# Optimization experiments

Measured on AMD Instinct MI355X. Metric: run time of the kernel, lower is better.

The kernel has to match this reference:

```python
import jax, jax.numpy as jnp
import numpy as np

H = 4          # global_attention_heads
NL = 32        # num_landmark_tokens
STRIDE = 16    # landmark_stride
D = 3072       # hidden_size
HD = D // H    # head_dim = 768
SCALE = 1.0 / np.sqrt(HD).astype(np.float32)


def _landmark_indices(seq_len: int) -> jnp.ndarray:
    # torch: arange(0, seq_len, stride); if >NL, index with linspace(0, n-1, NL).long() (truncation)
    idx = np.arange(0, seq_len, STRIDE, dtype=np.int64)
    if len(idx) > NL:
        sel = np.linspace(0, len(idx) - 1, NL).astype(np.int64)  # truncates like torch long cast
        idx = idx[sel]
    return jnp.asarray(idx)


def _attn(q_in, kv_in, Wq, bq, Wk, bk, Wv, bv, Wo, bo):
    # shared QKV/O projections, standard multi-head attention q_in -> kv_in
    B, Lq, _ = q_in.shape
    Lk = kv_in.shape[1]
    Q = (q_in @ Wq + bq).reshape(B, Lq, H, HD)
    K = (kv_in @ Wk + bk).reshape(B, Lk, H, HD)
    V = (kv_in @ Wv + bv).reshape(B, Lk, H, HD)
    scores = jnp.einsum('bqhd,bkhd->bhqk', Q, K) * SCALE
    w = jax.nn.softmax(scores, axis=-1)  # dropout is identity in eval
    ctx = jnp.einsum('bhqk,bkhd->bqhd', w, V).reshape(B, Lq, D)
    return ctx @ Wo + bo


def setup_inputs() -> dict:
    key = jax.random.key(0)
    ks = jax.random.split(key, 10)
    B, S = 2, 8192
    s = 1.0 / np.sqrt(D).astype(np.float32)
    return {
        'hidden_states': jax.random.normal(ks[0], (B, S, D), jnp.float32),
        'landmark_emb': jax.random.normal(ks[1], (NL, D), jnp.float32),
        'Wq': jax.random.normal(ks[2], (D, D), jnp.float32) * s,
        'bq': jnp.zeros((D,), jnp.float32),
        'Wk': jax.random.normal(ks[3], (D, D), jnp.float32) * s,
        'bk': jnp.zeros((D,), jnp.float32),
        'Wv': jax.random.normal(ks[4], (D, D), jnp.float32) * s,
        'bv': jnp.zeros((D,), jnp.float32),
        'Wo': jax.random.normal(ks[5], (D, D), jnp.float32) * s,
        'bo': jnp.zeros((D,), jnp.float32),
    }


def reference(hidden_states, landmark_emb, Wq, bq, Wk, bk, Wv, bv, Wo, bo):
    B, S, _ = hidden_states.shape
    li = _landmark_indices(S)  # [NL], static
    # gather landmarks + learned landmark embeddings
    landmark_tokens = hidden_states[:, li, :] + landmark_emb[None]  # [B, NL, D]
    # all tokens attend to 32 landmarks
    global_out = _attn(hidden_states, landmark_tokens, Wq, bq, Wk, bk, Wv, bv, Wo, bo)  # [B,S,D]
    # landmarks attend to all tokens
    landmark_out = _attn(landmark_tokens, hidden_states, Wq, bq, Wk, bk, Wv, bv, Wo, bo)  # [B,NL,D]
    # scatter landmark outputs back (index_copy-style, replaces python loop)
    updated = hidden_states.at[:, li, :].set(landmark_out)
    return updated + global_out
```

## Files before the change

kernel.cpp:

```cpp
#include <hip/hip_runtime.h>
#include <stdint.h>

#define S_LEN   8192
#define DMODEL  3072
#define HDIM    768
#define NLM     32
#define MTOK    16384
#define MV      16448
#define MP      16512
#define NQKV    9216
#define KDIM    3072
#define NKT     48
#define MTILES  64
#define SCALE_F 0.036084391824351615f

#define OFF_A    ((size_t)0)
#define OFF_WT   ((size_t)101449728)
#define OFF_QKV  ((size_t)176947200)
#define OFF_CTX  ((size_t)480116736)
#define OFF_BCAT ((size_t)581566464)
#define OFF_PART ((size_t)581615616)
#define OFF_KT   (OFF_PART)
#define OFF_VT   (OFF_PART + 393216)
#define OFF_ML2  (OFF_PART + 786432)
#define OFF_LMP  (OFF_PART + 917504)
#define OFF_CP   (OFF_A)

#if defined(__has_builtin)
#if __has_builtin(__builtin_amdgcn_global_load_lds)
#define USE_GLL 1
#endif
#endif
#ifndef USE_GLL
#define USE_GLL 0
#endif

typedef __attribute__((ext_vector_type(8))) short bf8_t;
typedef __attribute__((ext_vector_type(4))) float f4_t;
typedef __attribute__((ext_vector_type(4))) short s4_t;
typedef __attribute__((ext_vector_type(4))) unsigned short us4_t;

__device__ __forceinline__ float b2f(unsigned short u) {
  unsigned x = ((unsigned)u) << 16;
  float f;
  __builtin_memcpy(&f, &x, 4);
  return f;
}
__device__ __forceinline__ unsigned short f2b(float f) {
  unsigned x;
  __builtin_memcpy(&x, &f, 4);
  x += 0x7fffu + ((x >> 16) & 1u);
  return (unsigned short)(x >> 16);
}
__device__ __forceinline__ void load12(const unsigned short* p, float* f) {
  s4_t v0 = *(const s4_t*)p;
  s4_t v1 = *(const s4_t*)(p + 4);
  s4_t v2 = *(const s4_t*)(p + 8);
#pragma unroll
  for (int e = 0; e < 4; ++e) {
    f[e]     = b2f((unsigned short)v0[e]);
    f[4 + e] = b2f((unsigned short)v1[e]);
    f[8 + e] = b2f((unsigned short)v2[e]);
  }
}
__device__ __forceinline__ void store12(unsigned short* p, const float* f) {
  us4_t a = {f2b(f[0]), f2b(f[1]), f2b(f[2]), f2b(f[3])};
  us4_t b = {f2b(f[4]), f2b(f[5]), f2b(f[6]), f2b(f[7])};
  us4_t c = {f2b(f[8]), f2b(f[9]), f2b(f[10]), f2b(f[11])};
  *(us4_t*)p = a;
  *(us4_t*)(p + 4) = b;
  *(us4_t*)(p + 8) = c;
}

__global__ __launch_bounds__(256) void build_bcat(const float* __restrict__ bq,
                                                  const float* __restrict__ bk,
                                                  const float* __restrict__ bv,
                                                  const float* __restrict__ bo,
                                                  float* __restrict__ bcat) {
  int n = blockIdx.x * 256 + threadIdx.x;
  float v = (n < 3072) ? bq[n] : (n < 6144) ? bk[n - 3072]
          : (n < 9216) ? bv[n - 6144] : bo[n - 9216];
  bcat[n] = v;
}

__global__ __launch_bounds__(256) void build_a(const float* __restrict__ hs,
                                               const float* __restrict__ lemb,
                                               unsigned short* __restrict__ A) {
  size_t idx = (size_t)blockIdx.x * 256 + threadIdx.x;
  size_t e = idx * 4;
  int row = (int)(e / DMODEL);
  int col = (int)(e - (size_t)row * DMODEL);
  f4_t v;
  if (row < MTOK) {
    v = *(const f4_t*)(hs + e);
  } else if (row < MV) {
    int r2 = row - MTOK;
    int b = r2 >> 5, j = r2 & 31;
    int sel = (j * 511) / 31;
    int li = sel * 16;
    f4_t a = *(const f4_t*)(hs + ((size_t)(b * S_LEN + li)) * DMODEL + col);
    f4_t c = *(const f4_t*)(lemb + (size_t)j * DMODEL + col);
    v = a + c;
  } else {
    v = (f4_t){0.f, 0.f, 0.f, 0.f};
  }
  us4_t o = {f2b(v[0]), f2b(v[1]), f2b(v[2]), f2b(v[3])};
  *(us4_t*)(A + e) = o;
}

__global__ __launch_bounds__(256) void wtrans4(const float* __restrict__ W0,
                                               const float* __restrict__ W1,
                                               const float* __restrict__ W2,
                                               const float* __restrict__ W3,
                                               unsigned short* __restrict__ Wt) {
  __shared__ float t[32][33];
  const float* Wsel[4] = {W0, W1, W2, W3};
  const float* W = Wsel[blockIdx.z];
  unsigned short* dst = Wt + (size_t)blockIdx.z * 3072 * KDIM;
  int n0 = blockIdx.x * 32, k0 = blockIdx.y * 32;
  int x = threadIdx.x, y = threadIdx.y;
#pragma unroll
  for (int i = 0; i < 4; ++i)
    t[y + i * 8][x] = W[(size_t)(k0 + y + i * 8) * DMODEL + n0 + x];
  __syncthreads();
#pragma unroll
  for (int i = 0; i < 4; ++i)
    dst[(size_t)(n0 + y + i * 8) * DMODEL + k0 + x] = f2b(t[x][y + i * 8]);
}

__global__ __launch_bounds__(256) void lm_gemm_part(const unsigned short* __restrict__ A64,
                                                    const unsigned short* __restrict__ Bt,
                                                    float* __restrict__ part,
                                                    int N) {
  int wid = blockIdx.x * 4 + (threadIdx.x >> 6);
  int lane = threadIdx.x & 63;
  int row16 = lane & 15, quad = lane >> 4;
  int strips = N >> 5;
  int ks = wid / strips;
  int n0 = (wid - ks * strips) * 32;

  f4_t acc[4][2];
#pragma unroll
  for (int mi = 0; mi < 4; ++mi) {
    acc[mi][0] = (f4_t){0.f, 0.f, 0.f, 0.f};
    acc[mi][1] = (f4_t){0.f, 0.f, 0.f, 0.f};
  }
#pragma unroll 4
  for (int kt = ks * 16; kt < ks * 16 + 16; ++kt) {
    int k = kt * 32 + quad * 8;
    bf8_t b0 = *(const bf8_t*)(Bt + (size_t)(n0 + row16) * KDIM + k);
    bf8_t b1 = *(const bf8_t*)(Bt + (size_t)(n0 + 16 + row16) * KDIM + k);
#pragma unroll
    for (int mi = 0; mi < 4; ++mi) {
      bf8_t a = *(const bf8_t*)(A64 + (size_t)(mi * 16 + row16) * KDIM + k);
      acc[mi][0] = __builtin_amdgcn_mfma_f32_16x16x32_bf16(a, b0, acc[mi][0], 0, 0, 0);
      acc[mi][1] = __builtin_amdgcn_mfma_f32_16x16x32_bf16(a, b1, acc[mi][1], 0, 0, 0);
    }
  }
#pragma unroll
  for (int mi = 0; mi < 4; ++mi)
#pragma unroll
    for (int i = 0; i < 4; ++i) {
      int r = mi * 16 + quad * 4 + i;
#pragma unroll
      for (int nl = 0; nl < 2; ++nl) {
        int col = n0 + nl * 16 + row16;
        part[((size_t)ks * 64 + r) * N + col] = acc[mi][nl][i];
      }
    }
}

__global__ __launch_bounds__(256) void lm_gemm_fix(const float* __restrict__ part,
                                                   const float* __restrict__ bias,
                                                   unsigned short* __restrict__ C64,
                                                   int N) {
  int idx = blockIdx.x * 256 + threadIdx.x;
  int nq = N >> 2;
  int r = idx / nq;
  int c4 = (idx - r * nq) * 4;
  if (r >= 64) return;
  f4_t s = *(const f4_t*)(part + (size_t)r * N + c4);
#pragma unroll
  for (int ks = 1; ks < 6; ++ks)
    s += *(const f4_t*)(part + ((size_t)ks * 64 + r) * N + c4);
  f4_t bb = *(const f4_t*)(bias + c4);
  s += bb;
  us4_t o = {f2b(s[0]), f2b(s[1]), f2b(s[2]), f2b(s[3])};
  *(us4_t*)(C64 + (size_t)r * N + c4) = o;
}

#if USE_GLL
#define GLL16(SRC, OFF)                                                        \
  __builtin_amdgcn_global_load_lds(                                           \
      (const __attribute__((address_space(1))) void*)(SRC),                   \
      (__attribute__((address_space(3))) void*)(lds + (OFF)), 16, 0, 0)
#else
#define GLL16(SRC, OFF)                                                        \
  (*(bf8_t*)(lds + (OFF) + (unsigned)(threadIdx.x & 63) * 16) = *(const bf8_t*)(SRC))
#endif

#define STG_A(TT, KH, DD)                                                      \
  do {                                                                         \
    const unsigned short* _s = gA0 + (size_t)(TT) * 64 + (KH) * 32;            \
    GLL16(_s, (unsigned)((DD) * 32768 + (KH) * 16384) + wl16);                 \
    GLL16(_s + (size_t)128 * KDIM,                                             \
          (unsigned)((DD) * 32768 + (KH) * 16384 + 8192) + wl16);              \
  } while (0)
#define STG_B(TT, KH, DD)                                                      \
  do {                                                                         \
    const unsigned short* _s = gB0 + (size_t)(TT) * 64 + (KH) * 32;            \
    GLL16(_s, (unsigned)(65536 + (DD) * 32768 + (KH) * 16384) + wl16);         \
    GLL16(_s + (size_t)128 * KDIM,                                             \
          (unsigned)(65536 + (DD) * 32768 + (KH) * 16384 + 8192) + wl16);      \
  } while (0)

#define LDA8(DD, KH, QM, MI)                                                   \
  (*(const bf8_t*)(lds + (DD) * 32768 + (KH) * 16384 + aBase + (QM) * 4096 +   \
                   (MI) * 1024))
#define LDB8(DD, KH, NI)                                                       \
  (*(const bf8_t*)(lds + (DD) * 32768 + (KH) * 16384 + bBase + (NI) * 1024))

#define MFMA16(Q, A0, A1, A2, A3, B0, B1, B2, B3)                              \
  do {                                                                         \
    __builtin_amdgcn_s_setprio(1);                                             \
    acc[(Q)+0][0] = __builtin_amdgcn_mfma_f32_16x16x32_bf16(A0, B0, acc[(Q)+0][0], 0, 0, 0); \
    acc[(Q)+1][0] = __builtin_amdgcn_mfma_f32_16x16x32_bf16(A1, B0, acc[(Q)+1][0], 0, 0, 0); \
    acc[(Q)+2][0] = __builtin_amdgcn_mfma_f32_16x16x32_bf16(A2, B0, acc[(Q)+2][0], 0, 0, 0); \
    acc[(Q)+3][0] = __builtin_amdgcn_mfma_f32_16x16x32_bf16(A3, B0, acc[(Q)+3][0], 0, 0, 0); \
    acc[(Q)+0][1] = __builtin_amdgcn_mfma_f32_16x16x32_bf16(A0, B1, acc[(Q)+0][1], 0, 0, 0); \
    acc[(Q)+1][1] = __builtin_amdgcn_mfma_f32_16x16x32_bf16(A1, B1, acc[(Q)+1][1], 0, 0, 0); \
    acc[(Q)+2][1] = __builtin_amdgcn_mfma_f32_16x16x32_bf16(A2, B1, acc[(Q)+2][1], 0, 0, 0); \
    acc[(Q)+3][1] = __builtin_amdgcn_mfma_f32_16x16x32_bf16(A3, B1, acc[(Q)+3][1], 0, 0, 0); \
    acc[(Q)+0][2] = __builtin_amdgcn_mfma_f32_16x16x32_bf16(A0, B2, acc[(Q)+0][2], 0, 0, 0); \
    acc[(Q)+1][2] = __builtin_amdgcn_mfma_f32_16x16x32_bf16(A1, B2, acc[(Q)+1][2], 0, 0, 0); \
    acc[(Q)+2][2] = __builtin_amdgcn_mfma_f32_16x16x32_bf16(A2, B2, acc[(Q)+2][2], 0, 0, 0); \
    acc[(Q)+3][2] = __builtin_amdgcn_mfma_f32_16x16x32_bf16(A3, B2, acc[(Q)+3][2], 0, 0, 0); \
    acc[(Q)+0][3] = __builtin_amdgcn_mfma_f32_16x16x32_bf16(A0, B3, acc[(Q)+0][3], 0, 0, 0); \
    acc[(Q)+1][3] = __builtin_amdgcn_mfma_f32_16x16x32_bf16(A1, B3, acc[(Q)+1][3], 0, 0, 0); \
    acc[(Q)+2][3] = __builtin_amdgcn_mfma_f32_16x16x32_bf16(A2, B3, acc[(Q)+2][3], 0, 0, 0); \
    acc[(Q)+3][3] = __builtin_amdgcn_mfma_f32_16x16x32_bf16(A3, B3, acc[(Q)+3][3], 0, 0, 0); \
    __builtin_amdgcn_s_setprio(0);                                             \
  } while (0)

__global__ __launch_bounds__(512, 2) void gemm256(const unsigned short* __restrict__ A,
                                                  const unsigned short* __restrict__ Bt,
                                                  const float* __restrict__ bias,
                                                  unsigned short* __restrict__ C,
                                                  int N, int Ntiles) {
  extern __shared__ char lds[];
  const int tid = threadIdx.x;
  const int lane = tid & 63;
  const int wave = tid >> 6;
  const int WM = wave >> 2;
  const int WN = wave & 3;
  const int row16 = lane & 15, quad = lane >> 4;

  int nwg = (int)gridDim.x;
  int orig = (int)blockIdx.x;
  int q = nwg >> 3, r = nwg & 7;
  int xcd = orig & 7, lin = orig >> 3;
  int wg = (xcd < r ? xcd * (q + 1) : r * (q + 1) + (xcd - r) * q) + lin;

  int g = wg / (MTILES * 8);
  int w2 = wg - g * (MTILES * 8);
  int Ng = Ntiles - g * 8;
  int m_, nl;
  if (Ng >= 8) { m_ = w2 >> 3; nl = w2 & 7; }
  else         { m_ = w2 / Ng; nl = w2 - m_ * Ng; }
  const int tileM = m_ * 256;
  const int tileN = (g * 8 + nl) * 256;

  const int srow2 = tid >> 2;
  const int scq = (tid & 3) ^ ((srow2 >> 1) & 3);
  const unsigned short* gA0 = A + (size_t)(tileM + srow2) * KDIM + scq * 8;
  const unsigned short* gB0 = Bt + (size_t)(tileN + srow2) * KDIM + scq * 8;
  const unsigned wl16 = (unsigned)(tid & 448) * 16;

  const unsigned co = (unsigned)((quad * 16) ^ (((row16 >> 1) & 3) << 4));
  const unsigned aBase = (unsigned)(WM * 8192 + row16 * 64) + co;
  const unsigned bBase = 65536u + (unsigned)(WN * 4096 + row16 * 64) + co;

  f4_t acc[8][4];
#pragma unroll
  for (int a = 0; a < 8; ++a)
#pragma unroll
    for (int b = 0; b < 4; ++b) acc[a][b] = (f4_t){0.f, 0.f, 0.f, 0.f};

  STG_B(0, 0, 0); STG_A(0, 0, 0); STG_B(0, 1, 0); STG_A(0, 1, 0);
  STG_B(1, 0, 1); STG_A(1, 0, 1); STG_B(1, 1, 1);
  asm volatile("s_waitcnt vmcnt(6)" ::: "memory");
  __builtin_amdgcn_s_barrier();

#pragma unroll 2
  for (int t = 0; t < NKT; ++t) {
    const int d = t & 1;
    {
      bf8_t a0 = LDA8(d, 0, 0, 0), a1 = LDA8(d, 0, 0, 1),
            a2 = LDA8(d, 0, 0, 2), a3 = LDA8(d, 0, 0, 3);
      bf8_t b0 = LDB8(d, 0, 0), b1 = LDB8(d, 0, 1),
            b2 = LDB8(d, 0, 2), b3 = LDB8(d, 0, 3);
      if (t + 1 < NKT) STG_A(t + 1, 1, d ^ 1);
      __builtin_amdgcn_s_barrier();
      asm volatile("s_waitcnt lgkmcnt(0)");
      MFMA16(0, a0, a1, a2, a3, b0, b1, b2, b3);
      __builtin_amdgcn_s_barrier();
      bf8_t a4 = LDA8(d, 0, 1, 0), a5 = LDA8(d, 0, 1, 1),
            a6 = LDA8(d, 0, 1, 2), a7 = LDA8(d, 0, 1, 3);
      if (t + 2 < NKT) STG_B(t + 2, 0, d);
      __builtin_amdgcn_s_barrier();
      asm volatile("s_waitcnt lgkmcnt(0)");
      MFMA16(4, a4, a5, a6, a7, b0, b1, b2, b3);
      __builtin_amdgcn_s_barrier();
    }
    {
      bf8_t a0 = LDA8(d, 1, 0, 0), a1 = LDA8(d, 1, 0, 1),
            a2 = LDA8(d, 1, 0, 2), a3 = LDA8(d, 1, 0, 3);
      bf8_t b0 = LDB8(d, 1, 0), b1 = LDB8(d, 1, 1),
            b2 = LDB8(d, 1, 2), b3 = LDB8(d, 1, 3);
      if (t + 2 < NKT) STG_A(t + 2, 0, d);
      __builtin_amdgcn_s_barrier();
      asm volatile("s_waitcnt lgkmcnt(0)");
      MFMA16(0, a0, a1, a2, a3, b0, b1, b2, b3);
      __builtin_amdgcn_s_barrier();
      bf8_t a4 = LDA8(d, 1, 1, 0), a5 = LDA8(d, 1, 1, 1),
            a6 = LDA8(d, 1, 1, 2), a7 = LDA8(d, 1, 1, 3);
      if (t + 2 < NKT) STG_B(t + 2, 1, d);
      __builtin_amdgcn_s_barrier();
      asm volatile("s_waitcnt lgkmcnt(0)");
      MFMA16(4, a4, a5, a6, a7, b0, b1, b2, b3);
      if (t + 2 < NKT) asm volatile("s_waitcnt vmcnt(6)" ::: "memory");
      else             asm volatile("s_waitcnt vmcnt(0)" ::: "memory");
      __builtin_amdgcn_s_barrier();
    }
  }

  float bv_[4];
#pragma unroll
  for (int ni = 0; ni < 4; ++ni) bv_[ni] = bias[tileN + WN * 64 + ni * 16 + row16];
#pragma unroll
  for (int mi = 0; mi < 8; ++mi) {
#pragma unroll
    for (int i = 0; i < 4; ++i) {
      int grow = tileM + WM * 128 + mi * 16 + quad * 4 + i;
      size_t base = (size_t)grow * N + tileN + WN * 64 + row16;
#pragma unroll
      for (int ni = 0; ni < 4; ++ni)
        C[base + ni * 16] = f2b(acc[mi][ni][i] + bv_[ni]);
    }
  }
}

__global__ __launch_bounds__(256) void kv_prep(const unsigned short* __restrict__ QKV,
                                               unsigned short* __restrict__ KT,
                                               unsigned short* __restrict__ VT) {
  int idx = blockIdx.x * 256 + threadIdx.x;
  if (idx < 24576) {
    int bh = idx / 3072, i = idx % 3072;
    int b = bh >> 2, h = bh & 3;
    int j = i & 31, c = i >> 5;
    bf8_t v = *(const bf8_t*)(QKV + (size_t)(MTOK + b * NLM + j) * NQKV + DMODEL +
                              h * HDIM + c * 8);
    *(bf8_t*)(KT + (size_t)bh * 24576 + (size_t)(c * 32 + j) * 8) = v;
  } else {
    int i2 = idx - 24576;
    int bh = i2 / 3072, r = i2 % 3072;
    int b = bh >> 2, h = bh & 3;
    int d = r >> 2, slot = r & 3;
    unsigned short vals[8];
#pragma unroll
    for (int e = 0; e < 8; ++e)
      vals[e] = QKV[(size_t)(MTOK + b * NLM + slot * 8 + e) * NQKV + 2 * DMODEL +
                    h * HDIM + d];
    unsigned short* p = VT + (size_t)bh * 24576 + (size_t)d * 32 + slot * 8;
    *(us4_t*)p = (us4_t){vals[0], vals[1], vals[2], vals[3]};
    *(us4_t*)(p + 4) = (us4_t){vals[4], vals[5], vals[6], vals[7]};
  }
}

__global__ __launch_bounds__(256, 2) void glob_attn(const unsigned short* __restrict__ QKV,
                                                    const unsigned short* __restrict__ KT,
                                                    const unsigned short* __restrict__ VT,
                                                    unsigned short* __restrict__ CTX) {
  __shared__ unsigned short P_s[4][32][32];
  const int tid = threadIdx.x;
  const int lane = tid & 63;
  const int w = tid >> 6;
  const int row16 = lane & 15, quad = lane >> 4;

  const int qt = blockIdx.x & 63;
  const int h = (blockIdx.x >> 6) & 3;
  const int b = blockIdx.x >> 8;
  const int bh = b * 4 + h;
  const int rowbase = b * S_LEN + qt * 128 + w * 32;

  const unsigned short* KTb = KT + (size_t)bh * 24576;
  const unsigned short* VTb = VT + (size_t)bh * 24576;

  f4_t sc[2][2];
#pragma unroll
  for (int mi = 0; mi < 2; ++mi)
#pragma unroll
    for (int ni = 0; ni < 2; ++ni) sc[mi][ni] = (f4_t){0.f, 0.f, 0.f, 0.f};

#pragma unroll
  for (int kt = 0; kt < 24; ++kt) {
    bf8_t kb0 = *(const bf8_t*)(KTb + (size_t)((kt * 4 + quad) * 32 + row16) * 8);
    bf8_t kb1 = *(const bf8_t*)(KTb + (size_t)((kt * 4 + quad) * 32 + 16 + row16) * 8);
    bf8_t qa0 = *(const bf8_t*)(QKV + (size_t)(rowbase + row16) * NQKV + h * HDIM +
                                kt * 32 + quad * 8);
    bf8_t qa1 = *(const bf8_t*)(QKV + (size_t)(rowbase + 16 + row16) * NQKV + h * HDIM +
                                kt * 32 + quad * 8);
    sc[0][0] = __builtin_amdgcn_mfma_f32_16x16x32_bf16(qa0, kb0, sc[0][0], 0, 0, 0);
    sc[0][1] = __builtin_amdgcn_mfma_f32_16x16x32_bf16(qa0, kb1, sc[0][1], 0, 0, 0);
    sc[1][0] = __builtin_amdgcn_mfma_f32_16x16x32_bf16(qa1, kb0, sc[1][0], 0, 0, 0);
    sc[1][1] = __builtin_amdgcn_mfma_f32_16x16x32_bf16(qa1, kb1, sc[1][1], 0, 0, 0);
  }

#pragma unroll
  for (int mi = 0; mi < 2; ++mi) {
#pragma unroll
    for (int i = 0; i < 4; ++i) {
      float s0 = sc[mi][0][i] * SCALE_F;
      float s1 = sc[mi][1][i] * SCALE_F;
      float mx = fmaxf(s0, s1);
#pragma unroll
      for (int off = 8; off; off >>= 1) mx = fmaxf(mx, __shfl_xor(mx, off));
      float p0 = __expf(s0 - mx), p1 = __expf(s1 - mx);
      float sum = p0 + p1;
#pragma unroll
      for (int off = 8; off; off >>= 1) sum += __shfl_xor(sum, off);
      float inv = 1.f / sum;
      int rr = mi * 16 + quad * 4 + i;
      P_s[w][rr][row16] = f2b(p0 * inv);
      P_s[w][rr][16 + row16] = f2b(p1 * inv);
    }
  }
  __syncthreads();

  bf8_t pa0 = *(const bf8_t*)&P_s[w][row16][quad * 8];
  bf8_t pa1 = *(const bf8_t*)&P_s[w][16 + row16][quad * 8];
  unsigned short* ctxb = CTX + (size_t)rowbase * DMODEL + h * HDIM;

#pragma unroll
  for (int dch = 0; dch < 12; ++dch) {
    bf8_t vb[4];
#pragma unroll
    for (int ni = 0; ni < 4; ++ni)
      vb[ni] = *(const bf8_t*)(VTb + (size_t)(dch * 64 + ni * 16 + row16) * 32 + quad * 8);
#pragma unroll
    for (int mi = 0; mi < 2; ++mi) {
      bf8_t pa = mi ? pa1 : pa0;
#pragma unroll
      for (int ni = 0; ni < 4; ++ni) {
        f4_t c = __builtin_amdgcn_mfma_f32_16x16x32_bf16(
            pa, vb[ni], (f4_t){0.f, 0.f, 0.f, 0.f}, 0, 0, 0);
#pragma unroll
        for (int i = 0; i < 4; ++i)
          ctxb[(size_t)(mi * 16 + quad * 4 + i) * DMODEL + dch * 64 + ni * 16 + row16] =
              f2b(c[i]);
      }
    }
  }
}

__global__ __launch_bounds__(256, 2) void lm_attn_part(const unsigned short* __restrict__ QKV,
                                                       float* __restrict__ ctxpart,
                                                       float* __restrict__ mlpart) {
  int wid = blockIdx.x * 4 + (threadIdx.x >> 6);
  int lane = threadIdx.x & 63;
  int jg = wid & 3, kc = (wid >> 2) & 63, h = (wid >> 8) & 3, b = wid >> 10;

  float qreg[8][12];
#pragma unroll
  for (int jj = 0; jj < 8; ++jj)
    load12(QKV + (size_t)(MTOK + b * NLM + jg * 8 + jj) * NQKV + h * HDIM + lane * 12,
           qreg[jj]);

  float m[8], l[8], ctx[8][12];
#pragma unroll
  for (int jj = 0; jj < 8; ++jj) {
    m[jj] = -1e30f;
    l[jj] = 0.f;
#pragma unroll
    for (int e = 0; e < 12; ++e) ctx[jj][e] = 0.f;
  }

  for (int k = kc * 128; k < kc * 128 + 128; ++k) {
    size_t row = (size_t)(b * S_LEN + k);
    float kv[12], vv[12];
    load12(QKV + row * NQKV + DMODEL + h * HDIM + lane * 12, kv);
    float s[8];
#pragma unroll
    for (int jj = 0; jj < 8; ++jj) {
      float p = 0.f;
#pragma unroll
      for (int e = 0; e < 12; ++e) p += qreg[jj][e] * kv[e];
      s[jj] = p;
    }
#pragma unroll
    for (int jj = 0; jj < 8; ++jj) {
#pragma unroll
      for (int off = 32; off; off >>= 1) s[jj] += __shfl_xor(s[jj], off);
      s[jj] *= SCALE_F;
    }
    load12(QKV + row * NQKV + 2 * DMODEL + h * HDIM + lane * 12, vv);
#pragma unroll
    for (int jj = 0; jj < 8; ++jj) {
      if (s[jj] <= m[jj]) {
        float pp = __expf(s[jj] - m[jj]);
        l[jj] += pp;
#pragma unroll
        for (int e = 0; e < 12; ++e) ctx[jj][e] += pp * vv[e];
      } else {
        float al = __expf(m[jj] - s[jj]);
        m[jj] = s[jj];
        l[jj] = l[jj] * al + 1.f;
#pragma unroll
        for (int e = 0; e < 12; ++e) ctx[jj][e] = ctx[jj][e] * al + vv[e];
      }
    }
  }

#pragma unroll
  for (int jj = 0; jj < 8; ++jj) {
    int p = (((b * 4 + h) * 32) + (jg * 8 + jj)) * 64 + kc;
    float* cp = ctxpart + (size_t)p * HDIM + lane * 12;
#pragma unroll
    for (int e = 0; e < 12; ++e) cp[e] = ctx[jj][e];
    if (lane == 0) {
      mlpart[p * 2] = m[jj];
      mlpart[p * 2 + 1] = l[jj];
    }
  }
}

__global__ __launch_bounds__(256) void lm_combine(const float* __restrict__ ctxpart,
                                                  const float* __restrict__ mlpart,
                                                  unsigned short* __restrict__ CTX) {
  int wid = blockIdx.x * 4 + (threadIdx.x >> 6);
  int lane = threadIdx.x & 63;
  int j = wid & 31, h = (wid >> 5) & 3, b = wid >> 7;
  int base = wid * 64;
  float mk = mlpart[(base + lane) * 2];
  float lk = mlpart[(base + lane) * 2 + 1];
  float mm = mk;
#pragma unroll
  for (int off = 32; off; off >>= 1) mm = fmaxf(mm, __shfl_xor(mm, off));
  float al = __expf(mk - mm);
  float ls = al * lk;
#pragma unroll
  for (int off = 32; off; off >>= 1) ls += __shfl_xor(ls, off);

  float ctx[12];
#pragma unroll
  for (int e = 0; e < 12; ++e) ctx[e] = 0.f;
  for (int kc = 0; kc < 64; ++kc) {
    float a = __shfl(al, kc);
    const float* cp = ctxpart + (size_t)(base + kc) * HDIM + lane * 12;
#pragma unroll
    for (int e = 0; e < 12; ++e) ctx[e] += a * cp[e];
  }
  float inv = 1.f / ls;
#pragma unroll
  for (int e = 0; e < 12; ++e) ctx[e] *= inv;
  store12(CTX + (size_t)(MTOK + b * NLM + j) * DMODEL + h * HDIM + lane * 12, ctx);
}

__global__ __launch_bounds__(256) void compose(const float* __restrict__ hs,
                                               const unsigned short* __restrict__ PROJ,
                                               float* __restrict__ out) {
  size_t idx = (size_t)blockIdx.x * 256 + threadIdx.x;
  size_t e = idx * 4;
  int row = (int)(e / DMODEL);
  int col = (int)(e - (size_t)row * DMODEL);
  int b = row >> 13, s = row & (S_LEN - 1);

  us4_t g4 = *(const us4_t*)(PROJ + (size_t)row * DMODEL + col);
  int j = -1;
  if ((s & 15) == 0) {
    int sel = s >> 4;
    int jc = (sel * 31 + 510) / 511;
    if (jc < 32 && (jc * 511) / 31 == sel) j = jc;
  }
  f4_t base;
  if (j >= 0) {
    us4_t l4 = *(const us4_t*)(PROJ + (size_t)(MTOK + b * NLM + j) * DMODEL + col);
    base = (f4_t){b2f(l4[0]), b2f(l4[1]), b2f(l4[2]), b2f(l4[3])};
  } else {
    base = *(const f4_t*)(hs + e);
  }
  f4_t o = {base[0] + b2f(g4[0]), base[1] + b2f(g4[1]),
            base[2] + b2f(g4[2]), base[3] + b2f(g4[3])};
  *(f4_t*)(out + e) = o;
}

extern "C" void kernel_launch(void* const* d_in, const int* in_sizes, int n_in,
                              void* d_out, int out_size, void* d_ws, size_t ws_size,
                              hipStream_t stream) {
  const float* hs   = (const float*)d_in[0];
  const float* lemb = (const float*)d_in[1];
  const float* Wq   = (const float*)d_in[2];
  const float* bq   = (const float*)d_in[3];
  const float* Wk   = (const float*)d_in[4];
  const float* bk   = (const float*)d_in[5];
  const float* Wv   = (const float*)d_in[6];
  const float* bv   = (const float*)d_in[7];
  const float* Wo   = (const float*)d_in[8];
  const float* bo   = (const float*)d_in[9];
  float* out = (float*)d_out;
  char* ws = (char*)d_ws;

  unsigned short* A    = (unsigned short*)(ws + OFF_A);
  unsigned short* Wt   = (unsigned short*)(ws + OFF_WT);
  unsigned short* QKV  = (unsigned short*)(ws + OFF_QKV);
  unsigned short* CTX  = (unsigned short*)(ws + OFF_CTX);
  float*          bcat = (float*)(ws + OFF_BCAT);
  unsigned short* KT   = (unsigned short*)(ws + OFF_KT);
  unsigned short* VT   = (unsigned short*)(ws + OFF_VT);
  float*          ml   = (float*)(ws + OFF_ML2);
  float*          lmp  = (float*)(ws + OFF_LMP);
  float*          cpart= (float*)(ws + OFF_CP);
  unsigned short* PROJ = (unsigned short*)(ws + OFF_A);

  static bool attr_set = false;
  if (!attr_set) {
    (void)hipFuncSetAttribute(reinterpret_cast<const void*>(gemm256),
                              hipFuncAttributeMaxDynamicSharedMemorySize, 131072);
    attr_set = true;
  }

  build_bcat<<<dim3(48), dim3(256), 0, stream>>>(bq, bk, bv, bo, bcat);
  build_a<<<dim3(49536), dim3(256), 0, stream>>>(hs, lemb, A);
  wtrans4<<<dim3(96, 96, 4), dim3(32, 8), 0, stream>>>(Wq, Wk, Wv, Wo, Wt);

  gemm256<<<dim3(64 * 36), dim3(512), 131072, stream>>>(A, Wt, bcat, QKV, NQKV, 36);
  lm_gemm_part<<<dim3(432), dim3(256), 0, stream>>>(
      A + (size_t)MTOK * KDIM, Wt, lmp, NQKV);
  lm_gemm_fix<<<dim3(576), dim3(256), 0, stream>>>(
      lmp, bcat, QKV + (size_t)MTOK * NQKV, NQKV);

  kv_prep<<<dim3(192), dim3(256), 0, stream>>>(QKV, KT, VT);
  glob_attn<<<dim3(512), dim3(256), 0, stream>>>(QKV, KT, VT, CTX);
  lm_attn_part<<<dim3(512), dim3(256), 0, stream>>>(QKV, cpart, ml);
  lm_combine<<<dim3(64), dim3(256), 0, stream>>>(cpart, ml, CTX);

  lm_gemm_part<<<dim3(144), dim3(256), 0, stream>>>(
      CTX + (size_t)MTOK * DMODEL, Wt + (size_t)9216 * KDIM, lmp, DMODEL);
  lm_gemm_fix<<<dim3(192), dim3(256), 0, stream>>>(
      lmp, bcat + 9216, PROJ + (size_t)MTOK * DMODEL, DMODEL);

  gemm256<<<dim3(64 * 12), dim3(512), 131072, stream>>>(
      CTX, Wt + (size_t)9216 * KDIM, bcat + 9216, PROJ, DMODEL, 12);

  compose<<<dim3(49152), dim3(256), 0, stream>>>(hs, PROJ, out);
}
```

Measured before the change: 1.914 ms.

## Merge prep kernels, fold kv_prep into lm_gemm_fix, fuse attention launches

Three preprocessing kernels (bias concat, A build, weight transpose) become one launch that dispatches on block index. The K/V transposition from kv_prep is folded into the landmark GEMM fixup epilogue, and the global and landmark attention kernels share a single launch. The compose kernel also handles 8 elements per thread. The aim is to cut launch overhead and tail idle time between small kernels. The cost is a larger heterogeneous prep grid and scalar strided VT stores in the fixup.

```diff
diff --git a/kernel.cpp b/kernel.cpp
--- a/kernel.cpp
+++ b/kernel.cpp
@@ -72,53 +72,61 @@
   *(us4_t*)(p + 8) = c;
 }
 
-__global__ __launch_bounds__(256) void build_bcat(const float* __restrict__ bq,
-                                                  const float* __restrict__ bk,
-                                                  const float* __restrict__ bv,
-                                                  const float* __restrict__ bo,
-                                                  float* __restrict__ bcat) {
-  int n = blockIdx.x * 256 + threadIdx.x;
-  float v = (n < 3072) ? bq[n] : (n < 6144) ? bk[n - 3072]
-          : (n < 9216) ? bv[n - 6144] : bo[n - 9216];
-  bcat[n] = v;
-}
-
-__global__ __launch_bounds__(256) void build_a(const float* __restrict__ hs,
-                                               const float* __restrict__ lemb,
-                                               unsigned short* __restrict__ A) {
-  size_t idx = (size_t)blockIdx.x * 256 + threadIdx.x;
-  size_t e = idx * 4;
-  int row = (int)(e / DMODEL);
-  int col = (int)(e - (size_t)row * DMODEL);
-  f4_t v;
-  if (row < MTOK) {
-    v = *(const f4_t*)(hs + e);
-  } else if (row < MV) {
-    int r2 = row - MTOK;
-    int b = r2 >> 5, j = r2 & 31;
-    int sel = (j * 511) / 31;
-    int li = sel * 16;
-    f4_t a = *(const f4_t*)(hs + ((size_t)(b * S_LEN + li)) * DMODEL + col);
-    f4_t c = *(const f4_t*)(lemb + (size_t)j * DMODEL + col);
-    v = a + c;
-  } else {
-    v = (f4_t){0.f, 0.f, 0.f, 0.f};
-  }
-  us4_t o = {f2b(v[0]), f2b(v[1]), f2b(v[2]), f2b(v[3])};
-  *(us4_t*)(A + e) = o;
-}
-
-__global__ __launch_bounds__(256) void wtrans4(const float* __restrict__ W0,
-                                               const float* __restrict__ W1,
-                                               const float* __restrict__ W2,
-                                               const float* __restrict__ W3,
-                                               unsigned short* __restrict__ Wt) {
+__global__ __launch_bounds__(256) void prep(const float* __restrict__ hs,
+                                            const float* __restrict__ lemb,
+                                            const float* __restrict__ bq,
+                                            const float* __restrict__ bk,
+                                            const float* __restrict__ bv,
+                                            const float* __restrict__ bo,
+                                            const float* __restrict__ W0,
+                                            const float* __restrict__ W1,
+                                            const float* __restrict__ W2,
+                                            const float* __restrict__ W3,
+                                            unsigned short* __restrict__ A,
+                                            unsigned short* __restrict__ Wt,
+                                            float* __restrict__ bcat) {
   __shared__ float t[32][33];
+  int blk = blockIdx.x;
+  int tid = threadIdx.x;
+  if (blk < 48) {
+    int n = blk * 256 + tid;
+    float v = (n < 3072) ? bq[n] : (n < 6144) ? bk[n - 3072]
+            : (n < 9216) ? bv[n - 6144] : bo[n - 9216];
+    bcat[n] = v;
+    return;
+  }
+  if (blk < 48 + 49536) {
+    size_t idx = (size_t)(blk - 48) * 256 + tid;
+    size_t e = idx * 4;
+    int row = (int)(e / DMODEL);
+    int col = (int)(e - (size_t)row * DMODEL);
+    f4_t v;
+    if (row < MTOK) {
+      v = *(const f4_t*)(hs + e);
+    } else if (row < MV) {
+      int r2 = row - MTOK;
+      int b = r2 >> 5, j = r2 & 31;
+      int sel = (j * 511) / 31;
+      int li = sel * 16;
+      f4_t a = *(const f4_t*)(hs + ((size_t)(b * S_LEN + li)) * DMODEL + col);
+      f4_t c = *(const f4_t*)(lemb + (size_t)j * DMODEL + col);
+      v = a + c;
+    } else {
+      v = (f4_t){0.f, 0.f, 0.f, 0.f};
+    }
+    us4_t o = {f2b(v[0]), f2b(v[1]), f2b(v[2]), f2b(v[3])};
+    *(us4_t*)(A + e) = o;
+    return;
+  }
+  int i2 = blk - 49584;
+  int z = i2 / 9216;
+  int rem = i2 - z * 9216;
+  int by = rem / 96, bx = rem - by * 96;
   const float* Wsel[4] = {W0, W1, W2, W3};
-  const float* W = Wsel[blockIdx.z];
-  unsigned short* dst = Wt + (size_t)blockIdx.z * 3072 * KDIM;
-  int n0 = blockIdx.x * 32, k0 = blockIdx.y * 32;
-  int x = threadIdx.x, y = threadIdx.y;
+  const float* W = Wsel[z];
+  unsigned short* dst = Wt + (size_t)z * 3072 * KDIM;
+  int n0 = bx * 32, k0 = by * 32;
+  int x = tid & 31, y = tid >> 5;
 #pragma unroll
   for (int i = 0; i < 4; ++i)
     t[y + i * 8][x] = W[(size_t)(k0 + y + i * 8) * DMODEL + n0 + x];
@@ -173,7 +181,9 @@
 __global__ __launch_bounds__(256) void lm_gemm_fix(const float* __restrict__ part,
                                                    const float* __restrict__ bias,
                                                    unsigned short* __restrict__ C64,
-                                                   int N) {
+                                                   int N,
+                                                   unsigned short* __restrict__ KT,
+                                                   unsigned short* __restrict__ VT) {
   int idx = blockIdx.x * 256 + threadIdx.x;
   int nq = N >> 2;
   int r = idx / nq;
@@ -187,6 +197,23 @@
   s += bb;
   us4_t o = {f2b(s[0]), f2b(s[1]), f2b(s[2]), f2b(s[3])};
   *(us4_t*)(C64 + (size_t)r * N + c4) = o;
+
+  if (KT) {
+    int b = r >> 5, j = r & 31;
+    if (c4 >= 3072 && c4 < 6144) {
+      int cc = c4 - 3072;
+      int h = cc / 768, c0 = cc - h * 768;
+      int bh = b * 4 + h;
+      *(us4_t*)(KT + (size_t)bh * 24576 + ((size_t)(c0 >> 3) * 32 + j) * 8 + (c0 & 7)) = o;
+    } else if (c4 >= 6144) {
+      int cc = c4 - 6144;
+      int h = cc / 768, d0 = cc - h * 768;
+      int bh = b * 4 + h;
+      unsigned short* vt = VT + (size_t)bh * 24576 + (size_t)d0 * 32 + j;
+#pragma unroll
+      for (int k = 0; k < 4; ++k) vt[(size_t)k * 32] = (unsigned short)o[k];
+    }
+  }
 }
 
 #if USE_GLL
@@ -350,124 +377,97 @@
   }
 }
 
-__global__ __launch_bounds__(256) void kv_prep(const unsigned short* __restrict__ QKV,
-                                               unsigned short* __restrict__ KT,
-                                               unsigned short* __restrict__ VT) {
-  int idx = blockIdx.x * 256 + threadIdx.x;
-  if (idx < 24576) {
-    int bh = idx / 3072, i = idx % 3072;
-    int b = bh >> 2, h = bh & 3;
-    int j = i & 31, c = i >> 5;
-    bf8_t v = *(const bf8_t*)(QKV + (size_t)(MTOK + b * NLM + j) * NQKV + DMODEL +
-                              h * HDIM + c * 8);
-    *(bf8_t*)(KT + (size_t)bh * 24576 + (size_t)(c * 32 + j) * 8) = v;
-  } else {
-    int i2 = idx - 24576;
-    int bh = i2 / 3072, r = i2 % 3072;
-    int b = bh >> 2, h = bh & 3;
-    int d = r >> 2, slot = r & 3;
-    unsigned short vals[8];
-#pragma unroll
-    for (int e = 0; e < 8; ++e)
-      vals[e] = QKV[(size_t)(MTOK + b * NLM + slot * 8 + e) * NQKV + 2 * DMODEL +
-                    h * HDIM + d];
-    unsigned short* p = VT + (size_t)bh * 24576 + (size_t)d * 32 + slot * 8;
-    *(us4_t*)p = (us4_t){vals[0], vals[1], vals[2], vals[3]};
-    *(us4_t*)(p + 4) = (us4_t){vals[4], vals[5], vals[6], vals[7]};
-  }
-}
-
-__global__ __launch_bounds__(256, 2) void glob_attn(const unsigned short* __restrict__ QKV,
-                                                    const unsigned short* __restrict__ KT,
-                                                    const unsigned short* __restrict__ VT,
-                                                    unsigned short* __restrict__ CTX) {
+__global__ __launch_bounds__(256, 2) void attn_fused(const unsigned short* __restrict__ QKV,
+                                                     const unsigned short* __restrict__ KT,
+                                                     const unsigned short* __restrict__ VT,
+                                                     unsigned short* __restrict__ CTX,
+                                                     float* __restrict__ ctxpart,
+                                                     float* __restrict__ mlpart) {
   __shared__ unsigned short P_s[4][32][32];
   const int tid = threadIdx.x;
   const int lane = tid & 63;
-  const int w = tid >> 6;
   const int row16 = lane & 15, quad = lane >> 4;
 
-  const int qt = blockIdx.x & 63;
-  const int h = (blockIdx.x >> 6) & 3;
-  const int b = blockIdx.x >> 8;
-  const int bh = b * 4 + h;
-  const int rowbase = b * S_LEN + qt * 128 + w * 32;
-
-  const unsigned short* KTb = KT + (size_t)bh * 24576;
-  const unsigned short* VTb = VT + (size_t)bh * 24576;
-
-  f4_t sc[2][2];
-#pragma unroll
-  for (int mi = 0; mi < 2; ++mi)
-#pragma unroll
-    for (int ni = 0; ni < 2; ++ni) sc[mi][ni] = (f4_t){0.f, 0.f, 0.f, 0.f};
-
-#pragma unroll
-  for (int kt = 0; kt < 24; ++kt) {
-    bf8_t kb0 = *(const bf8_t*)(KTb + (size_t)((kt * 4 + quad) * 32 + row16) * 8);
-    bf8_t kb1 = *(const bf8_t*)(KTb + (size_t)((kt * 4 + quad) * 32 + 16 + row16) * 8);
-    bf8_t qa0 = *(const bf8_t*)(QKV + (size_t)(rowbase + row16) * NQKV + h * HDIM +
-                                kt * 32 + quad * 8);
-    bf8_t qa1 = *(const bf8_t*)(QKV + (size_t)(rowbase + 16 + row16) * NQKV + h * HDIM +
-                                kt * 32 + quad * 8);
-    sc[0][0] = __builtin_amdgcn_mfma_f32_16x16x32_bf16(qa0, kb0, sc[0][0], 0, 0, 0);
-    sc[0][1] = __builtin_amdgcn_mfma_f32_16x16x32_bf16(qa0, kb1, sc[0][1], 0, 0, 0);
-    sc[1][0] = __builtin_amdgcn_mfma_f32_16x16x32_bf16(qa1, kb0, sc[1][0], 0, 0, 0);
-    sc[1][1] = __builtin_amdgcn_mfma_f32_16x16x32_bf16(qa1, kb1, sc[1][1], 0, 0, 0);
-  }
-
-#pragma unroll
-  for (int mi = 0; mi < 2; ++mi) {
-#pragma unroll
-    for (int i = 0; i < 4; ++i) {
-      float s0 = sc[mi][0][i] * SCALE_F;
-      float s1 = sc[mi][1][i] * SCALE_F;
-      float mx = fmaxf(s0, s1);
-#pragma unroll
-      for (int off = 8; off; off >>= 1) mx = fmaxf(mx, __shfl_xor(mx, off));
-      float p0 = __expf(s0 - mx), p1 = __expf(s1 - mx);
-      float sum = p0 + p1;
-#pragma unroll
-      for (int off = 8; off; off >>= 1) sum += __shfl_xor(sum, off);
-      float inv = 1.f / sum;
-      int rr = mi * 16 + quad * 4 + i;
-      P_s[w][rr][row16] = f2b(p0 * inv);
-      P_s[w][rr][16 + row16] = f2b(p1 * inv);
-    }
-  }
-  __syncthreads();
-
-  bf8_t pa0 = *(const bf8_t*)&P_s[w][row16][quad * 8];
-  bf8_t pa1 = *(const bf8_t*)&P_s[w][16 + row16][quad * 8];
-  unsigned short* ctxb = CTX + (size_t)rowbase * DMODEL + h * HDIM;
-
-#pragma unroll
-  for (int dch = 0; dch < 12; ++dch) {
-    bf8_t vb[4];
-#pragma unroll
-    for (int ni = 0; ni < 4; ++ni)
-      vb[ni] = *(const bf8_t*)(VTb + (size_t)(dch * 64 + ni * 16 + row16) * 32 + quad * 8);
+  if (blockIdx.x < 512) {
+    const int w = tid >> 6;
+    const int qt = blockIdx.x & 63;
+    const int h = (blockIdx.x >> 6) & 3;
+    const int b = blockIdx.x >> 8;
+    const int bh = b * 4 + h;
+    const int rowbase = b * S_LEN + qt * 128 + w * 32;
+
+    const unsigned short* KTb = KT + (size_t)bh * 24576;
+    const unsigned short* VTb = VT + (size_t)bh * 24576;
+
+    f4_t sc[2][2];
+#pragma unroll
+    for (int mi = 0; mi < 2; ++mi)
+#pragma unroll
+      for (int ni = 0; ni < 2; ++ni) sc[mi][ni] = (f4_t){0.f, 0.f, 0.f, 0.f};
+
+#pragma unroll
+    for (int kt = 0; kt < 24; ++kt) {
+      bf8_t kb0 = *(const bf8_t*)(KTb + (size_t)((kt * 4 + quad) * 32 + row16) * 8);
+      bf8_t kb1 = *(const bf8_t*)(KTb + (size_t)((kt * 4 + quad) * 32 + 16 + row16) * 8);
+      bf8_t qa0 = *(const bf8_t*)(QKV + (size_t)(rowbase + row16) * NQKV + h * HDIM +
+                                  kt * 32 + quad * 8);
+      bf8_t qa1 = *(const bf8_t*)(QKV + (size_t)(rowbase + 16 + row16) * NQKV + h * HDIM +
+                                  kt * 32 + quad * 8);
+      sc[0][0] = __builtin_amdgcn_mfma_f32_16x16x32_bf16(qa0, kb0, sc[0][0], 0, 0, 0);
+      sc[0][1] = __builtin_amdgcn_mfma_f32_16x16x32_bf16(qa0, kb1, sc[0][1], 0, 0, 0);
+      sc[1][0] = __builtin_amdgcn_mfma_f32_16x16x32_bf16(qa1, kb0, sc[1][0], 0, 0, 0);
+      sc[1][1] = __builtin_amdgcn_mfma_f32_16x16x32_bf16(qa1, kb1, sc[1][1], 0, 0, 0);
+    }
+
 #pragma unroll
     for (int mi = 0; mi < 2; ++mi) {
-      bf8_t pa = mi ? pa1 : pa0;
-#pragma unroll
-      for (int ni = 0; ni < 4; ++ni) {
-        f4_t c = __builtin_amdgcn_mfma_f32_16x16x32_bf16(
-            pa, vb[ni], (f4_t){0.f, 0.f, 0.f, 0.f}, 0, 0, 0);
-#pragma unroll
-        for (int i = 0; i < 4; ++i)
-          ctxb[(size_t)(mi * 16 + quad * 4 + i) * DMODEL + dch * 64 + ni * 16 + row16] =
-              f2b(c[i]);
+#pragma unroll
+      for (int i = 0; i < 4; ++i) {
+        float s0 = sc[mi][0][i] * SCALE_F;
+        float s1 = sc[mi][1][i] * SCALE_F;
+        float mx = fmaxf(s0, s1);
+#pragma unroll
+        for (int off = 8; off; off >>= 1) mx = fmaxf(mx, __shfl_xor(mx, off));
+        float p0 = __expf(s0 - mx), p1 = __expf(s1 - mx);
+        float sum = p0 + p1;
+#pragma unroll
+        for (int off = 8; off; off >>= 1) sum += __shfl_xor(sum, off);
+        float inv = 1.f / sum;
+        int rr = mi * 16 + quad * 4 + i;
+        P_s[w][rr][row16] = f2b(p0 * inv);
+        P_s[w][rr][16 + row16] = f2b(p1 * inv);
       }
     }
-  }
-}
-
-__global__ __launch_bounds__(256, 2) void lm_attn_part(const unsigned short* __restrict__ QKV,
-                                                       float* __restrict__ ctxpart,
-                                                       float* __restrict__ mlpart) {
-  int wid = blockIdx.x * 4 + (threadIdx.x >> 6);
-  int lane = threadIdx.x & 63;
+    __syncthreads();
+
+    bf8_t pa0 = *(const bf8_t*)&P_s[w][row16][quad * 8];
+    bf8_t pa1 = *(const bf8_t*)&P_s[w][16 + row16][quad * 8];
+    unsigned short* ctxb = CTX + (size_t)rowbase * DMODEL + h * HDIM;
+
+#pragma unroll
+    for (int dch = 0; dch < 12; ++dch) {
+      bf8_t vb[4];
+#pragma unroll
+      for (int ni = 0; ni < 4; ++ni)
+        vb[ni] = *(const bf8_t*)(VTb + (size_t)(dch * 64 + ni * 16 + row16) * 32 + quad * 8);
+#pragma unroll
+      for (int mi = 0; mi < 2; ++mi) {
+        bf8_t pa = mi ? pa1 : pa0;
+#pragma unroll
+        for (int ni = 0; ni < 4; ++ni) {
+          f4_t c = __builtin_amdgcn_mfma_f32_16x16x32_bf16(
+              pa, vb[ni], (f4_t){0.f, 0.f, 0.f, 0.f}, 0, 0, 0);
+#pragma unroll
+          for (int i = 0; i < 4; ++i)
+            ctxb[(size_t)(mi * 16 + quad * 4 + i) * DMODEL + dch * 64 + ni * 16 + row16] =
+                f2b(c[i]);
+        }
+      }
+    }
+    return;
+  }
+
+  int wid = (blockIdx.x - 512) * 4 + (tid >> 6);
   int jg = wid & 3, kc = (wid >> 2) & 63, h = (wid >> 8) & 3, b = wid >> 10;
 
   float qreg[8][12];
@@ -570,28 +570,36 @@
                                                const unsigned short* __restrict__ PROJ,
                                                float* __restrict__ out) {
   size_t idx = (size_t)blockIdx.x * 256 + threadIdx.x;
-  size_t e = idx * 4;
+  size_t e = idx * 8;
   int row = (int)(e / DMODEL);
   int col = (int)(e - (size_t)row * DMODEL);
   int b = row >> 13, s = row & (S_LEN - 1);
 
-  us4_t g4 = *(const us4_t*)(PROJ + (size_t)row * DMODEL + col);
+  us4_t g4a = *(const us4_t*)(PROJ + (size_t)row * DMODEL + col);
+  us4_t g4b = *(const us4_t*)(PROJ + (size_t)row * DMODEL + col + 4);
   int j = -1;
   if ((s & 15) == 0) {
     int sel = s >> 4;
     int jc = (sel * 31 + 510) / 511;
     if (jc < 32 && (jc * 511) / 31 == sel) j = jc;
   }
-  f4_t base;
+  f4_t ba, bb;
   if (j >= 0) {
-    us4_t l4 = *(const us4_t*)(PROJ + (size_t)(MTOK + b * NLM + j) * DMODEL + col);
-    base = (f4_t){b2f(l4[0]), b2f(l4[1]), b2f(l4[2]), b2f(l4[3])};
+    const unsigned short* lp = PROJ + (size_t)(MTOK + b * NLM + j) * DMODEL + col;
+    us4_t l4a = *(const us4_t*)lp;
+    us4_t l4b = *(const us4_t*)(lp + 4);
+    ba = (f4_t){b2f(l4a[0]), b2f(l4a[1]), b2f(l4a[2]), b2f(l4a[3])};
+    bb = (f4_t){b2f(l4b[0]), b2f(l4b[1]), b2f(l4b[2]), b2f(l4b[3])};
   } else {
-    base = *(const f4_t*)(hs + e);
-  }
-  f4_t o = {base[0] + b2f(g4[0]), base[1] + b2f(g4[1]),
-            base[2] + b2f(g4[2]), base[3] + b2f(g4[3])};
-  *(f4_t*)(out + e) = o;
+    ba = *(const f4_t*)(hs + e);
+    bb = *(const f4_t*)(hs + e + 4);
+  }
+  f4_t oa = {ba[0] + b2f(g4a[0]), ba[1] + b2f(g4a[1]),
+             ba[2] + b2f(g4a[2]), ba[3] + b2f(g4a[3])};
+  f4_t ob = {bb[0] + b2f(g4b[0]), bb[1] + b2f(g4b[1]),
+             bb[2] + b2f(g4b[2]), bb[3] + b2f(g4b[3])};
+  *(f4_t*)(out + e) = oa;
+  *(f4_t*)(out + e + 4) = ob;
 }
 
 extern "C" void kernel_launch(void* const* d_in, const int* in_sizes, int n_in,
@@ -629,28 +637,25 @@
     attr_set = true;
   }
 
-  build_bcat<<<dim3(48), dim3(256), 0, stream>>>(bq, bk, bv, bo, bcat);
-  build_a<<<dim3(49536), dim3(256), 0, stream>>>(hs, lemb, A);
-  wtrans4<<<dim3(96, 96, 4), dim3(32, 8), 0, stream>>>(Wq, Wk, Wv, Wo, Wt);
+  prep<<<dim3(48 + 49536 + 36864), dim3(256), 0, stream>>>(
+      hs, lemb, bq, bk, bv, bo, Wq, Wk, Wv, Wo, A, Wt, bcat);
 
   gemm256<<<dim3(64 * 36), dim3(512), 131072, stream>>>(A, Wt, bcat, QKV, NQKV, 36);
   lm_gemm_part<<<dim3(432), dim3(256), 0, stream>>>(
       A + (size_t)MTOK * KDIM, Wt, lmp, NQKV);
   lm_gemm_fix<<<dim3(576), dim3(256), 0, stream>>>(
-      lmp, bcat, QKV + (size_t)MTOK * NQKV, NQKV);
-
-  kv_prep<<<dim3(192), dim3(256), 0, stream>>>(QKV, KT, VT);
-  glob_attn<<<dim3(512), dim3(256), 0, stream>>>(QKV, KT, VT, CTX);
-  lm_attn_part<<<dim3(512), dim3(256), 0, stream>>>(QKV, cpart, ml);
+      lmp, bcat, QKV + (size_t)MTOK * NQKV, NQKV, KT, VT);
+
+  attn_fused<<<dim3(1024), dim3(256), 0, stream>>>(QKV, KT, VT, CTX, cpart, ml);
   lm_combine<<<dim3(64), dim3(256), 0, stream>>>(cpart, ml, CTX);
 
   lm_gemm_part<<<dim3(144), dim3(256), 0, stream>>>(
       CTX + (size_t)MTOK * DMODEL, Wt + (size_t)9216 * KDIM, lmp, DMODEL);
   lm_gemm_fix<<<dim3(192), dim3(256), 0, stream>>>(
-      lmp, bcat + 9216, PROJ + (size_t)MTOK * DMODEL, DMODEL);
+      lmp, bcat + 9216, PROJ + (size_t)MTOK * DMODEL, DMODEL, nullptr, nullptr);
 
   gemm256<<<dim3(64 * 12), dim3(512), 131072, stream>>>(
       CTX, Wt + (size_t)9216 * KDIM, bcat + 9216, PROJ, DMODEL, 12);
 
-  compose<<<dim3(49152), dim3(256), 0, stream>>>(hs, PROJ, out);
-}
+  compose<<<dim3(24576), dim3(256), 0, stream>>>(hs, PROJ, out);
+}
```

Measured after the change: 1.916 ms (median of 3 runs). Within noise of the previous version (+0.1%).
